# Kernel optimization log

Hardware: AMD Instinct MI355X
Metric: run time of the kernel (lower is better)

Reference implementation:

```python
import jax, jax.numpy as jnp
import numpy as np

V = 32000      # vocab_size
E = 256        # ModelConfig.n_embed
T_BLOCK = 2048 # ModelConfig.block_size
H = 4          # n_head (hardcoded in Bigram)
L = 3          # number of Blocks
HS = E // H    # head_size
EPS = 1e-5

def _ln(x, g, b):
    mu = jnp.mean(x, axis=-1, keepdims=True)
    var = jnp.var(x, axis=-1, keepdims=True)
    return (x - mu) * jax.lax.rsqrt(var + EPS) * g + b

def setup_inputs() -> dict:
    key = jax.random.key(0)
    ks = jax.random.split(key, 16)
    s = 0.02
    inp = {
        "idx": jax.random.randint(ks[0], (4, T_BLOCK), 0, V),
        "tok_emb": jax.random.normal(ks[1], (V, E), jnp.float32) * s,
        "pos_emb": jax.random.normal(ks[2], (T_BLOCK, E), jnp.float32) * s,
        # per-layer stacked params (heads concatenated -> full ExE projections)
        "Wq": jax.random.normal(ks[3], (L, E, E), jnp.float32) * s,
        "Wk": jax.random.normal(ks[4], (L, E, E), jnp.float32) * s,
        "Wv": jax.random.normal(ks[5], (L, E, E), jnp.float32) * s,
        "Wproj": jax.random.normal(ks[6], (L, E, E), jnp.float32) * s,
        "bproj": jnp.zeros((L, E), jnp.float32),
        "ln1_g": jnp.ones((L, E), jnp.float32),
        "ln1_b": jnp.zeros((L, E), jnp.float32),
        "W1": jax.random.normal(ks[7], (L, E, 4 * E), jnp.float32) * s,
        "b1": jnp.zeros((L, 4 * E), jnp.float32),
        "W2": jax.random.normal(ks[8], (L, 4 * E, E), jnp.float32) * s,
        "b2": jnp.zeros((L, E), jnp.float32),
        "ln2_g": jnp.ones((L, E), jnp.float32),
        "ln2_b": jnp.zeros((L, E), jnp.float32),
        "Wlm": jax.random.normal(ks[9], (E, V), jnp.float32) * s,
        "blm": jnp.zeros((V,), jnp.float32),
    }
    return inp

def reference(idx, tok_emb, pos_emb, Wq, Wk, Wv, Wproj, bproj, ln1_g, ln1_b,
              W1, b1, W2, b2, ln2_g, ln2_b, Wlm, blm):
    B, T = idx.shape
    x = tok_emb[idx] + pos_emb[:T]  # [B,T,E]
    causal = jnp.tril(jnp.ones((T, T), bool))
    # NOTE: source scales by C**0.5 with C = n_embed (not head_size)
    scale = 1.0 / jnp.sqrt(jnp.float32(E))
    for l in range(L):
        h = _ln(x, ln1_g[l], ln1_b[l])
        q = (h @ Wq[l]).reshape(B, T, H, HS).transpose(0, 2, 1, 3)
        k = (h @ Wk[l]).reshape(B, T, H, HS).transpose(0, 2, 1, 3)
        v = (h @ Wv[l]).reshape(B, T, H, HS).transpose(0, 2, 1, 3)
        wei = jnp.einsum('bhtd,bhsd->bhts', q, k) * scale
        wei = jnp.where(causal, wei, -jnp.inf)
        wei = jax.nn.softmax(wei, axis=-1)
        y = jnp.einsum('bhts,bhsd->bhtd', wei, v)
        y = y.transpose(0, 2, 1, 3).reshape(B, T, E)
        x = x + y @ Wproj[l] + bproj[l]
        h2 = _ln(x, ln2_g[l], ln2_b[l])
        x = x + jax.nn.relu(h2 @ W1[l] + b1[l]) @ W2[l] + b2[l]
    # ln_f exists in __init__ but is never applied in forward — skipped.
    logits = x @ Wlm + blm  # [B,T,V]
    return logits
```

## Files before the change

### kernel.cpp

```cpp
#include <hip/hip_runtime.h>
#include <hip/hip_bf16.h>

#define EMB 256
#define NHEAD 4
#define HSZ 64
#define NLAYER 3
#define TBLK 2048
#define VOCAB 32000
#define BATCH 4
#define LNEPS 1e-5f
#define BT (BATCH * TBLK)
#define QKVD (3 * EMB)

typedef __attribute__((ext_vector_type(8))) short bf16x8v;
typedef __attribute__((ext_vector_type(4))) float f32x4;
typedef unsigned short u16;
typedef unsigned int u32;

__device__ __forceinline__ u16 f2bf(float f) {
    union { float f; u32 u; } c; c.f = f;
    u32 r = c.u + 0x7fff + ((c.u >> 16) & 1);
    return (u16)(r >> 16);
}
__device__ __forceinline__ u32 pack2(float a, float b) {
    return (u32)f2bf(a) | ((u32)f2bf(b) << 16);
}

__global__ __launch_bounds__(64) void embed_kernel(
    const int* __restrict__ idx, const float* __restrict__ tok,
    const float* __restrict__ pos, float* __restrict__ x)
{
    const int row = blockIdx.x;
    const int t = row & (TBLK - 1);
    const int token = idx[row];
    const int e = threadIdx.x * 4;
    const float4 tv = *(const float4*)&tok[(size_t)token * EMB + e];
    const float4 pv = *(const float4*)&pos[(size_t)t * EMB + e];
    float4 o;
    o.x = tv.x + pv.x; o.y = tv.y + pv.y; o.z = tv.z + pv.z; o.w = tv.w + pv.w;
    *(float4*)&x[(size_t)row * EMB + e] = o;
}

__global__ __launch_bounds__(64) void ln_kernel(
    const float* __restrict__ x, const float* __restrict__ g,
    const float* __restrict__ b, u16* __restrict__ out)
{
    const int row = blockIdx.x;
    const int e = threadIdx.x * 4;
    const float4 xv = *(const float4*)&x[(size_t)row * EMB + e];
    float s1 = xv.x + xv.y + xv.z + xv.w;
    float s2 = xv.x * xv.x + xv.y * xv.y + xv.z * xv.z + xv.w * xv.w;
    #pragma unroll
    for (int off = 32; off >= 1; off >>= 1) {
        s1 += __shfl_xor(s1, off);
        s2 += __shfl_xor(s2, off);
    }
    const float mu  = s1 * (1.0f / EMB);
    const float var = s2 * (1.0f / EMB) - mu * mu;
    const float rs  = rsqrtf(var + LNEPS);
    const float4 gv = *(const float4*)&g[e];
    const float4 bv = *(const float4*)&b[e];
    ushort4 o;
    o.x = f2bf((xv.x - mu) * rs * gv.x + bv.x);
    o.y = f2bf((xv.y - mu) * rs * gv.y + bv.y);
    o.z = f2bf((xv.z - mu) * rs * gv.z + bv.z);
    o.w = f2bf((xv.w - mu) * rs * gv.w + bv.w);
    *(ushort4*)&out[(size_t)row * EMB + e] = o;
}

__global__ __launch_bounds__(256) void cast_kernel(
    const float* __restrict__ in, u16* __restrict__ out)
{
    const int i = (blockIdx.x * 256 + threadIdx.x) * 4;
    const float4 v = *(const float4*)&in[i];
    ushort4 o; o.x = f2bf(v.x); o.y = f2bf(v.y); o.z = f2bf(v.z); o.w = f2bf(v.w);
    *(ushort4*)&out[i] = o;
}

__global__ __launch_bounds__(256) void transpose_cast(
    const float* __restrict__ W, u16* __restrict__ Wt, int K, int N,
    size_t sW, size_t sWt)
{
    __shared__ float t[32][33];
    W  += (size_t)blockIdx.z * sW;
    Wt += (size_t)blockIdx.z * sWt;
    const int bx = blockIdx.x, by = blockIdx.y;
    const int tx = threadIdx.x, ty = threadIdx.y;
    #pragma unroll
    for (int i = 0; i < 32; i += 8)
        t[ty + i][tx] = W[(size_t)(by * 32 + ty + i) * N + bx * 32 + tx];
    __syncthreads();
    #pragma unroll
    for (int i = 0; i < 32; i += 8)
        Wt[(size_t)(bx * 32 + ty + i) * K + by * 32 + tx] = f2bf(t[tx][ty + i]);
}

template<int BNT, int BIAS, int RES, int RELU, int OUTBF>
__global__ __launch_bounds__(256) void mgemm(
    const u16* __restrict__ A, const u16* __restrict__ Bt,
    const float* __restrict__ bias, const float* __restrict__ res,
    void* __restrict__ Cv, int M, int N, int K)
{
    constexpr int LDW = 40;
    constexpr int MI = (BNT == 128) ? 4 : 2;
    __shared__ u16 Al[2][128 * LDW];
    __shared__ u16 Bl[2][BNT * LDW];
    const int tid = threadIdx.x;
    const int bm = blockIdx.x, bn = blockIdx.y;
    const int wid = tid >> 6, lane = tid & 63;
    const int wr = (BNT == 128) ? (wid >> 1) * 64 : wid * 32;
    const int wc = (BNT == 128) ? (wid & 1) * 64 : 0;
    const int fr = lane & 15, fq = lane >> 4;

    const int sra = tid >> 1,                       ska = (tid & 1) * 16;
    const int srb = (BNT == 128) ? (tid >> 1) : (tid >> 2);
    const int skb = (BNT == 128) ? (tid & 1) * 16 : (tid & 3) * 8;

    const u16* Ag = A + (size_t)(bm * 128 + sra) * K + ska;
    const u16* Bg = Bt + (size_t)(bn * BNT + srb) * K + skb;

    bf16x8v a0 = *(const bf16x8v*)Ag;
    bf16x8v a1 = *(const bf16x8v*)(Ag + 8);
    bf16x8v b0 = *(const bf16x8v*)Bg;
    bf16x8v b1 = (BNT == 128) ? *(const bf16x8v*)(Bg + 8) : b0;

    f32x4 acc[MI][4];
    #pragma unroll
    for (int i = 0; i < MI; ++i)
        #pragma unroll
        for (int j = 0; j < 4; ++j)
            acc[i][j] = f32x4{0.f, 0.f, 0.f, 0.f};

    int buf = 0;
    for (int k0 = 0; k0 < K; k0 += 32, buf ^= 1) {
        u16* Aw = &Al[buf][sra * LDW + ska];
        *(bf16x8v*)Aw = a0; *(bf16x8v*)(Aw + 8) = a1;
        u16* Bw = &Bl[buf][srb * LDW + skb];
        *(bf16x8v*)Bw = b0;
        if (BNT == 128) *(bf16x8v*)(Bw + 8) = b1;
        __syncthreads();
        if (k0 + 32 < K) {
            a0 = *(const bf16x8v*)(Ag + k0 + 32);
            a1 = *(const bf16x8v*)(Ag + k0 + 40);
            b0 = *(const bf16x8v*)(Bg + k0 + 32);
            if (BNT == 128) b1 = *(const bf16x8v*)(Bg + k0 + 40);
        }
        bf16x8v af[MI], bfr[4];
        #pragma unroll
        for (int mi = 0; mi < MI; ++mi)
            af[mi] = *(const bf16x8v*)&Al[buf][(wr + mi * 16 + fr) * LDW + fq * 8];
        #pragma unroll
        for (int ni = 0; ni < 4; ++ni)
            bfr[ni] = *(const bf16x8v*)&Bl[buf][(wc + ni * 16 + fr) * LDW + fq * 8];
        #pragma unroll
        for (int mi = 0; mi < MI; ++mi)
            #pragma unroll
            for (int ni = 0; ni < 4; ++ni)
                acc[mi][ni] = __builtin_amdgcn_mfma_f32_16x16x32_bf16(
                    af[mi], bfr[ni], acc[mi][ni], 0, 0, 0);
    }

    float* Cf = (float*)Cv;
    u16*   Cb = (u16*)Cv;
    #pragma unroll
    for (int mi = 0; mi < MI; ++mi) {
        #pragma unroll
        for (int j = 0; j < 4; ++j) {
            const int r = bm * 128 + wr + mi * 16 + fq * 4 + j;
            #pragma unroll
            for (int ni = 0; ni < 4; ++ni) {
                const int c = bn * BNT + wc + ni * 16 + fr;
                float v = acc[mi][ni][j];
                if (BIAS) v += bias[c];
                if (RELU) v = fmaxf(v, 0.f);
                if (RES)  v += res[(size_t)r * N + c];
                if (OUTBF) Cb[(size_t)r * N + c] = f2bf(v);
                else       Cf[(size_t)r * N + c] = v;
            }
        }
    }
}

__global__ __launch_bounds__(256) void attn_kernel(
    const u16* __restrict__ qkv, u16* __restrict__ y)
{
    constexpr int LDK = 72;
    __shared__ u16 Kl[2][64 * LDK];
    __shared__ u16 Vt[2][64 * LDK];

    const int tid = threadIdx.x;
    const int qt = (int)gridDim.x - 1 - (int)blockIdx.x;
    const int bh = blockIdx.y;
    const int b = bh >> 2, h = bh & 3;
    const int w = tid >> 6, lane = tid & 63;
    const int fr = lane & 15, fq = lane >> 4;
    const size_t rowbase = (size_t)b * TBLK;
    const int qoff = h * HSZ, koff = EMB + h * HSZ, voff = 2 * EMB + h * HSZ;
    const int qg = qt * 64 + w * 16 + fr;

    bf16x8v qf[2];
    #pragma unroll
    for (int ks = 0; ks < 2; ++ks)
        qf[ks] = *(const bf16x8v*)&qkv[(rowbase + qg) * QKVD + qoff + ks * 32 + fq * 8];

    f32x4 yac[4];
    #pragma unroll
    for (int mi = 0; mi < 4; ++mi) yac[mi] = f32x4{0.f, 0.f, 0.f, 0.f};
    float m = -1e30f, l = 0.f;

    const int skv = tid >> 2, sc = (tid & 3) * 16;
    const u16* kbase = &qkv[(rowbase + skv) * QKVD + koff + sc];
    const u16* vbase = &qkv[(rowbase + skv) * QKVD + voff + sc];

    bf16x8v kr0 = *(const bf16x8v*)kbase;
    bf16x8v kr1 = *(const bf16x8v*)(kbase + 8);
    bf16x8v vr0 = *(const bf16x8v*)vbase;
    bf16x8v vr1 = *(const bf16x8v*)(vbase + 8);

    int buf = 0;
    for (int kv0 = 0; kv0 <= qt * 64; kv0 += 64, buf ^= 1) {
        {
            u16* Kw = &Kl[buf][skv * LDK + sc];
            *(bf16x8v*)Kw = kr0; *(bf16x8v*)(Kw + 8) = kr1;
            #pragma unroll
            for (int i = 0; i < 8; ++i) Vt[buf][(sc + i) * LDK + skv] = (u16)vr0[i];
            #pragma unroll
            for (int i = 0; i < 8; ++i) Vt[buf][(sc + 8 + i) * LDK + skv] = (u16)vr1[i];
        }
        __syncthreads();
        if (kv0 + 64 <= qt * 64) {
            const size_t off = (size_t)(kv0 + 64) * QKVD;
            kr0 = *(const bf16x8v*)(kbase + off);
            kr1 = *(const bf16x8v*)(kbase + off + 8);
            vr0 = *(const bf16x8v*)(vbase + off);
            vr1 = *(const bf16x8v*)(vbase + off + 8);
        }

        f32x4 st[4];
        #pragma unroll
        for (int mb = 0; mb < 4; ++mb) {
            st[mb] = f32x4{0.f, 0.f, 0.f, 0.f};
            #pragma unroll
            for (int ks = 0; ks < 2; ++ks) {
                const bf16x8v kf = *(const bf16x8v*)
                    &Kl[buf][(mb * 16 + fr) * LDK + ks * 32 + fq * 8];
                st[mb] = __builtin_amdgcn_mfma_f32_16x16x32_bf16(
                    kf, qf[ks], st[mb], 0, 0, 0);
            }
        }
        float p[4][4];
        float mloc = -1e30f;
        #pragma unroll
        for (int mb = 0; mb < 4; ++mb)
            #pragma unroll
            for (int j = 0; j < 4; ++j) {
                const int kvg = kv0 + mb * 16 + fq * 4 + j;
                const float s = (kvg <= qg) ? st[mb][j] * 0.0625f : -1e30f;
                p[mb][j] = s;
                mloc = fmaxf(mloc, s);
            }
        mloc = fmaxf(mloc, __shfl_xor(mloc, 16));
        mloc = fmaxf(mloc, __shfl_xor(mloc, 32));
        const float mnew = fmaxf(m, mloc);
        const float alpha = __expf(m - mnew);
        float rsum = 0.f;
        #pragma unroll
        for (int mb = 0; mb < 4; ++mb)
            #pragma unroll
            for (int j = 0; j < 4; ++j) {
                p[mb][j] = __expf(p[mb][j] - mnew);
                rsum += p[mb][j];
            }
        rsum += __shfl_xor(rsum, 16);
        rsum += __shfl_xor(rsum, 32);
        l = l * alpha + rsum;
        m = mnew;
        #pragma unroll
        for (int mi = 0; mi < 4; ++mi) yac[mi] *= alpha;

        u32 pk[4][2];
        #pragma unroll
        for (int mb = 0; mb < 4; ++mb) {
            pk[mb][0] = pack2(p[mb][0], p[mb][1]);
            pk[mb][1] = pack2(p[mb][2], p[mb][3]);
        }
        #pragma unroll
        for (int ksv = 0; ksv < 2; ++ksv) {
            union { u32 u[4]; bf16x8v v; } pf;
            #pragma unroll
            for (int t = 0; t < 4; ++t) {
                const int srcl = ((fq & 1) * 2 + (t >> 1)) * 16 + fr;
                const u32 lo = __shfl(pk[ksv * 2 + 0][t & 1], srcl);
                const u32 hi = __shfl(pk[ksv * 2 + 1][t & 1], srcl);
                pf.u[t] = (fq >> 1) ? hi : lo;
            }
            #pragma unroll
            for (int mi = 0; mi < 4; ++mi) {
                const bf16x8v vf = *(const bf16x8v*)
                    &Vt[buf][(mi * 16 + fr) * LDK + ksv * 32 + fq * 8];
                yac[mi] = __builtin_amdgcn_mfma_f32_16x16x32_bf16(
                    vf, pf.v, yac[mi], 0, 0, 0);
            }
        }
    }

    const float inv = 1.f / l;
    #pragma unroll
    for (int mi = 0; mi < 4; ++mi) {
        ushort4 o;
        o.x = f2bf(yac[mi][0] * inv);
        o.y = f2bf(yac[mi][1] * inv);
        o.z = f2bf(yac[mi][2] * inv);
        o.w = f2bf(yac[mi][3] * inv);
        *(ushort4*)&y[(rowbase + qg) * EMB + h * HSZ + mi * 16 + fq * 4] = o;
    }
}

extern "C" void kernel_launch(void* const* d_in, const int* in_sizes, int n_in,
                              void* d_out, int out_size, void* d_ws, size_t ws_size,
                              hipStream_t stream) {
    const int*   idx   = (const int*)  d_in[0];
    const float* tok   = (const float*)d_in[1];
    const float* pos   = (const float*)d_in[2];
    const float* Wq    = (const float*)d_in[3];
    const float* Wk    = (const float*)d_in[4];
    const float* Wv    = (const float*)d_in[5];
    const float* Wproj = (const float*)d_in[6];
    const float* bproj = (const float*)d_in[7];
    const float* ln1g  = (const float*)d_in[8];
    const float* ln1b  = (const float*)d_in[9];
    const float* W1    = (const float*)d_in[10];
    const float* b1    = (const float*)d_in[11];
    const float* W2    = (const float*)d_in[12];
    const float* b2    = (const float*)d_in[13];
    const float* ln2g  = (const float*)d_in[14];
    const float* ln2b  = (const float*)d_in[15];
    const float* Wlm   = (const float*)d_in[16];
    const float* blm   = (const float*)d_in[17];
    float* out = (float*)d_out;

    float* x    = (float*)d_ws;
    u16*   hb   = (u16*)(x + (size_t)BT * EMB);
    u16*   qkvb = hb + (size_t)BT * EMB;
    u16*   yb   = qkvb + (size_t)BT * QKVD;
    u16*   hid  = qkvb;
    u16*   Wqkvt  = yb + (size_t)BT * EMB;
    u16*   Wprojt = Wqkvt  + (size_t)NLAYER * QKVD * EMB;
    u16*   W1t    = Wprojt + (size_t)NLAYER * EMB * EMB;
    u16*   W2t    = W1t    + (size_t)NLAYER * EMB * 4 * EMB;
    u16*   Wlmt   = W2t    + (size_t)NLAYER * 4 * EMB * EMB;

    const dim3 tb(32, 8);
    transpose_cast<<<dim3(8, 8, NLAYER), tb, 0, stream>>>(
        Wq, Wqkvt, EMB, EMB, (size_t)EMB*EMB, (size_t)QKVD*EMB);
    transpose_cast<<<dim3(8, 8, NLAYER), tb, 0, stream>>>(
        Wk, Wqkvt + EMB*EMB, EMB, EMB, (size_t)EMB*EMB, (size_t)QKVD*EMB);
    transpose_cast<<<dim3(8, 8, NLAYER), tb, 0, stream>>>(
        Wv, Wqkvt + 2*EMB*EMB, EMB, EMB, (size_t)EMB*EMB, (size_t)QKVD*EMB);
    transpose_cast<<<dim3(8, 8, NLAYER), tb, 0, stream>>>(
        Wproj, Wprojt, EMB, EMB, (size_t)EMB*EMB, (size_t)EMB*EMB);
    transpose_cast<<<dim3(32, 8, NLAYER), tb, 0, stream>>>(
        W1, W1t, EMB, 4*EMB, (size_t)EMB*4*EMB, (size_t)EMB*4*EMB);
    transpose_cast<<<dim3(8, 32, NLAYER), tb, 0, stream>>>(
        W2, W2t, 4*EMB, EMB, (size_t)4*EMB*EMB, (size_t)4*EMB*EMB);
    transpose_cast<<<dim3(VOCAB/32, 8, 1), tb, 0, stream>>>(
        Wlm, Wlmt, EMB, VOCAB, 0, 0);

    embed_kernel<<<BT, 64, 0, stream>>>(idx, tok, pos, x);

    for (int l = 0; l < NLAYER; ++l) {
        ln_kernel<<<BT, 64, 0, stream>>>(x, ln1g + l*EMB, ln1b + l*EMB, hb);
        mgemm<128,0,0,0,1><<<dim3(BT/128, QKVD/128), 256, 0, stream>>>(
            hb, Wqkvt + (size_t)l*QKVD*EMB, nullptr, nullptr, qkvb, BT, QKVD, EMB);
        attn_kernel<<<dim3(TBLK/64, BATCH*NHEAD), 256, 0, stream>>>(qkvb, yb);
        mgemm<64,1,1,0,0><<<dim3(BT/128, EMB/64), 256, 0, stream>>>(
            yb, Wprojt + (size_t)l*EMB*EMB, bproj + l*EMB, x, x, BT, EMB, EMB);
        ln_kernel<<<BT, 64, 0, stream>>>(x, ln2g + l*EMB, ln2b + l*EMB, hb);
        mgemm<128,1,0,1,1><<<dim3(BT/128, 4*EMB/128), 256, 0, stream>>>(
            hb, W1t + (size_t)l*EMB*4*EMB, b1 + l*4*EMB, nullptr, hid, BT, 4*EMB, EMB);
        mgemm<64,1,1,0,0><<<dim3(BT/128, EMB/64), 256, 0, stream>>>(
            hid, W2t + (size_t)l*4*EMB*EMB, b2 + l*EMB, x, x, BT, EMB, 4*EMB);
    }

    cast_kernel<<<BT*EMB/1024, 256, 0, stream>>>(x, hb);
    mgemm<128,1,0,0,0><<<dim3(BT/128, VOCAB/128), 256, 0, stream>>>(
        hb, Wlmt, blm, nullptr, out, BT, VOCAB, EMB);
}
```

Baseline: 710.4 us.

## Use direct global-to-LDS loads in GEMM, add MFMA priority, fuse small launches

The GEMM staging now uses global_load_lds to copy A/B tiles straight into unpadded LDS, replacing the register round-trip and padded stores. MFMA sections in the GEMM and attention kernels are wrapped with s_setprio. Several small launches are merged: the QKV/proj weight transposes become one kernel, embed/LN pack four rows per block, and the final cast is folded into the last W2 GEMM with bf16 output. Dropping the LDS padding may bring back bank conflicts on fragment reads.

Result: no change. 701.0 us (-1.3%).

```diff
diff --git a/kernel.cpp b/kernel.cpp
--- a/kernel.cpp
+++ b/kernel.cpp
@@ -26,14 +26,20 @@
     return (u32)f2bf(a) | ((u32)f2bf(b) << 16);
 }
 
-__global__ __launch_bounds__(64) void embed_kernel(
+__device__ __forceinline__ void gload16(const u16* g, u16* l) {
+    __builtin_amdgcn_global_load_lds(
+        (__attribute__((address_space(1))) void*)g,
+        (__attribute__((address_space(3))) void*)l, 16, 0, 0);
+}
+
+__global__ __launch_bounds__(256) void embed_kernel(
     const int* __restrict__ idx, const float* __restrict__ tok,
     const float* __restrict__ pos, float* __restrict__ x)
 {
-    const int row = blockIdx.x;
+    const int row = blockIdx.x * 4 + (threadIdx.x >> 6);
     const int t = row & (TBLK - 1);
     const int token = idx[row];
-    const int e = threadIdx.x * 4;
+    const int e = (threadIdx.x & 63) * 4;
     const float4 tv = *(const float4*)&tok[(size_t)token * EMB + e];
     const float4 pv = *(const float4*)&pos[(size_t)t * EMB + e];
     float4 o;
@@ -41,12 +47,12 @@
     *(float4*)&x[(size_t)row * EMB + e] = o;
 }
 
-__global__ __launch_bounds__(64) void ln_kernel(
+__global__ __launch_bounds__(256) void ln_kernel(
     const float* __restrict__ x, const float* __restrict__ g,
     const float* __restrict__ b, u16* __restrict__ out)
 {
-    const int row = blockIdx.x;
-    const int e = threadIdx.x * 4;
+    const int row = blockIdx.x * 4 + (threadIdx.x >> 6);
+    const int e = (threadIdx.x & 63) * 4;
     const float4 xv = *(const float4*)&x[(size_t)row * EMB + e];
     float s1 = xv.x + xv.y + xv.z + xv.w;
     float s2 = xv.x * xv.x + xv.y * xv.y + xv.z * xv.z + xv.w * xv.w;
@@ -68,15 +74,6 @@
     *(ushort4*)&out[(size_t)row * EMB + e] = o;
 }
 
-__global__ __launch_bounds__(256) void cast_kernel(
-    const float* __restrict__ in, u16* __restrict__ out)
-{
-    const int i = (blockIdx.x * 256 + threadIdx.x) * 4;
-    const float4 v = *(const float4*)&in[i];
-    ushort4 o; o.x = f2bf(v.x); o.y = f2bf(v.y); o.z = f2bf(v.z); o.w = f2bf(v.w);
-    *(ushort4*)&out[i] = o;
-}
-
 __global__ __launch_bounds__(256) void transpose_cast(
     const float* __restrict__ W, u16* __restrict__ Wt, int K, int N,
     size_t sW, size_t sWt)
@@ -95,16 +92,41 @@
         Wt[(size_t)(bx * 32 + ty + i) * K + by * 32 + tx] = f2bf(t[tx][ty + i]);
 }
 
+__global__ __launch_bounds__(256) void transpose_qkvp(
+    const float* __restrict__ Wq, const float* __restrict__ Wk,
+    const float* __restrict__ Wv, const float* __restrict__ Wp,
+    u16* __restrict__ Wqkvt, u16* __restrict__ Wprojt)
+{
+    __shared__ float t[32][33];
+    const int which = blockIdx.z & 3, l = blockIdx.z >> 2;
+    const float* W;
+    u16* Wt;
+    switch (which) {
+        case 0: W = Wq + (size_t)l*EMB*EMB; Wt = Wqkvt + (size_t)l*QKVD*EMB;               break;
+        case 1: W = Wk + (size_t)l*EMB*EMB; Wt = Wqkvt + (size_t)l*QKVD*EMB + EMB*EMB;     break;
+        case 2: W = Wv + (size_t)l*EMB*EMB; Wt = Wqkvt + (size_t)l*QKVD*EMB + 2*EMB*EMB;   break;
+        default:W = Wp + (size_t)l*EMB*EMB; Wt = Wprojt + (size_t)l*EMB*EMB;               break;
+    }
+    const int bx = blockIdx.x, by = blockIdx.y;
+    const int tx = threadIdx.x, ty = threadIdx.y;
+    #pragma unroll
+    for (int i = 0; i < 32; i += 8)
+        t[ty + i][tx] = W[(size_t)(by * 32 + ty + i) * EMB + bx * 32 + tx];
+    __syncthreads();
+    #pragma unroll
+    for (int i = 0; i < 32; i += 8)
+        Wt[(size_t)(bx * 32 + ty + i) * EMB + by * 32 + tx] = f2bf(t[tx][ty + i]);
+}
+
 template<int BNT, int BIAS, int RES, int RELU, int OUTBF>
 __global__ __launch_bounds__(256) void mgemm(
     const u16* __restrict__ A, const u16* __restrict__ Bt,
     const float* __restrict__ bias, const float* __restrict__ res,
     void* __restrict__ Cv, int M, int N, int K)
 {
-    constexpr int LDW = 40;
     constexpr int MI = (BNT == 128) ? 4 : 2;
-    __shared__ u16 Al[2][128 * LDW];
-    __shared__ u16 Bl[2][BNT * LDW];
+    __shared__ u16 Al[2][128 * 32];
+    __shared__ u16 Bl[2][BNT * 32];
     const int tid = threadIdx.x;
     const int bm = blockIdx.x, bn = blockIdx.y;
     const int wid = tid >> 6, lane = tid & 63;
@@ -112,17 +134,10 @@
     const int wc = (BNT == 128) ? (wid & 1) * 64 : 0;
     const int fr = lane & 15, fq = lane >> 4;
 
-    const int sra = tid >> 1,                       ska = (tid & 1) * 16;
-    const int srb = (BNT == 128) ? (tid >> 1) : (tid >> 2);
-    const int skb = (BNT == 128) ? (tid & 1) * 16 : (tid & 3) * 8;
-
-    const u16* Ag = A + (size_t)(bm * 128 + sra) * K + ska;
-    const u16* Bg = Bt + (size_t)(bn * BNT + srb) * K + skb;
-
-    bf16x8v a0 = *(const bf16x8v*)Ag;
-    bf16x8v a1 = *(const bf16x8v*)(Ag + 8);
-    bf16x8v b0 = *(const bf16x8v*)Bg;
-    bf16x8v b1 = (BNT == 128) ? *(const bf16x8v*)(Bg + 8) : b0;
+    const int l4 = lane >> 2, lc = (lane & 3) * 8;
+    const u16* Aga = A  + (size_t)(bm * 128 + wid * 16 + l4) * K + lc;
+    const u16* Bga = Bt + (size_t)(bn * BNT + wid * 16 + l4) * K + lc;
+    const int lin = (wid * 16 + l4) * 32 + lc;
 
     f32x4 acc[MI][4];
     #pragma unroll
@@ -131,33 +146,36 @@
         for (int j = 0; j < 4; ++j)
             acc[i][j] = f32x4{0.f, 0.f, 0.f, 0.f};
 
+    gload16(Aga,                  &Al[0][lin]);
+    gload16(Aga + (size_t)64 * K, &Al[0][lin + 64 * 32]);
+    gload16(Bga,                  &Bl[0][lin]);
+    if (BNT == 128) gload16(Bga + (size_t)64 * K, &Bl[0][lin + 64 * 32]);
+
     int buf = 0;
     for (int k0 = 0; k0 < K; k0 += 32, buf ^= 1) {
-        u16* Aw = &Al[buf][sra * LDW + ska];
-        *(bf16x8v*)Aw = a0; *(bf16x8v*)(Aw + 8) = a1;
-        u16* Bw = &Bl[buf][srb * LDW + skb];
-        *(bf16x8v*)Bw = b0;
-        if (BNT == 128) *(bf16x8v*)(Bw + 8) = b1;
         __syncthreads();
         if (k0 + 32 < K) {
-            a0 = *(const bf16x8v*)(Ag + k0 + 32);
-            a1 = *(const bf16x8v*)(Ag + k0 + 40);
-            b0 = *(const bf16x8v*)(Bg + k0 + 32);
-            if (BNT == 128) b1 = *(const bf16x8v*)(Bg + k0 + 40);
+            gload16(Aga + k0 + 32,                  &Al[buf ^ 1][lin]);
+            gload16(Aga + (size_t)64 * K + k0 + 32, &Al[buf ^ 1][lin + 64 * 32]);
+            gload16(Bga + k0 + 32,                  &Bl[buf ^ 1][lin]);
+            if (BNT == 128)
+                gload16(Bga + (size_t)64 * K + k0 + 32, &Bl[buf ^ 1][lin + 64 * 32]);
         }
         bf16x8v af[MI], bfr[4];
         #pragma unroll
         for (int mi = 0; mi < MI; ++mi)
-            af[mi] = *(const bf16x8v*)&Al[buf][(wr + mi * 16 + fr) * LDW + fq * 8];
+            af[mi] = *(const bf16x8v*)&Al[buf][(wr + mi * 16 + fr) * 32 + fq * 8];
         #pragma unroll
         for (int ni = 0; ni < 4; ++ni)
-            bfr[ni] = *(const bf16x8v*)&Bl[buf][(wc + ni * 16 + fr) * LDW + fq * 8];
+            bfr[ni] = *(const bf16x8v*)&Bl[buf][(wc + ni * 16 + fr) * 32 + fq * 8];
+        __builtin_amdgcn_s_setprio(1);
         #pragma unroll
         for (int mi = 0; mi < MI; ++mi)
             #pragma unroll
             for (int ni = 0; ni < 4; ++ni)
                 acc[mi][ni] = __builtin_amdgcn_mfma_f32_16x16x32_bf16(
                     af[mi], bfr[ni], acc[mi][ni], 0, 0, 0);
+        __builtin_amdgcn_s_setprio(0);
     }
 
     float* Cf = (float*)Cv;
@@ -237,6 +255,7 @@
         }
 
         f32x4 st[4];
+        __builtin_amdgcn_s_setprio(1);
         #pragma unroll
         for (int mb = 0; mb < 4; ++mb) {
             st[mb] = f32x4{0.f, 0.f, 0.f, 0.f};
@@ -248,6 +267,7 @@
                     kf, qf[ks], st[mb], 0, 0, 0);
             }
         }
+        __builtin_amdgcn_s_setprio(0);
         float p[4][4];
         float mloc = -1e30f;
         #pragma unroll
@@ -294,6 +314,7 @@
                 const u32 hi = __shfl(pk[ksv * 2 + 1][t & 1], srcl);
                 pf.u[t] = (fq >> 1) ? hi : lo;
             }
+            __builtin_amdgcn_s_setprio(1);
             #pragma unroll
             for (int mi = 0; mi < 4; ++mi) {
                 const bf16x8v vf = *(const bf16x8v*)
@@ -301,6 +322,7 @@
                 yac[mi] = __builtin_amdgcn_mfma_f32_16x16x32_bf16(
                     vf, pf.v, yac[mi], 0, 0, 0);
             }
+            __builtin_amdgcn_s_setprio(0);
         }
     }
 
@@ -351,14 +373,8 @@
     u16*   Wlmt   = W2t    + (size_t)NLAYER * 4 * EMB * EMB;
 
     const dim3 tb(32, 8);
-    transpose_cast<<<dim3(8, 8, NLAYER), tb, 0, stream>>>(
-        Wq, Wqkvt, EMB, EMB, (size_t)EMB*EMB, (size_t)QKVD*EMB);
-    transpose_cast<<<dim3(8, 8, NLAYER), tb, 0, stream>>>(
-        Wk, Wqkvt + EMB*EMB, EMB, EMB, (size_t)EMB*EMB, (size_t)QKVD*EMB);
-    transpose_cast<<<dim3(8, 8, NLAYER), tb, 0, stream>>>(
-        Wv, Wqkvt + 2*EMB*EMB, EMB, EMB, (size_t)EMB*EMB, (size_t)QKVD*EMB);
-    transpose_cast<<<dim3(8, 8, NLAYER), tb, 0, stream>>>(
-        Wproj, Wprojt, EMB, EMB, (size_t)EMB*EMB, (size_t)EMB*EMB);
+    transpose_qkvp<<<dim3(8, 8, NLAYER * 4), tb, 0, stream>>>(
+        Wq, Wk, Wv, Wproj, Wqkvt, Wprojt);
     transpose_cast<<<dim3(32, 8, NLAYER), tb, 0, stream>>>(
         W1, W1t, EMB, 4*EMB, (size_t)EMB*4*EMB, (size_t)EMB*4*EMB);
     transpose_cast<<<dim3(8, 32, NLAYER), tb, 0, stream>>>(
@@ -366,23 +382,27 @@
     transpose_cast<<<dim3(VOCAB/32, 8, 1), tb, 0, stream>>>(
         Wlm, Wlmt, EMB, VOCAB, 0, 0);
 
-    embed_kernel<<<BT, 64, 0, stream>>>(idx, tok, pos, x);
+    embed_kernel<<<BT/4, 256, 0, stream>>>(idx, tok, pos, x);
 
     for (int l = 0; l < NLAYER; ++l) {
-        ln_kernel<<<BT, 64, 0, stream>>>(x, ln1g + l*EMB, ln1b + l*EMB, hb);
+        ln_kernel<<<BT/4, 256, 0, stream>>>(x, ln1g + l*EMB, ln1b + l*EMB, hb);
         mgemm<128,0,0,0,1><<<dim3(BT/128, QKVD/128), 256, 0, stream>>>(
             hb, Wqkvt + (size_t)l*QKVD*EMB, nullptr, nullptr, qkvb, BT, QKVD, EMB);
         attn_kernel<<<dim3(TBLK/64, BATCH*NHEAD), 256, 0, stream>>>(qkvb, yb);
         mgemm<64,1,1,0,0><<<dim3(BT/128, EMB/64), 256, 0, stream>>>(
             yb, Wprojt + (size_t)l*EMB*EMB, bproj + l*EMB, x, x, BT, EMB, EMB);
-        ln_kernel<<<BT, 64, 0, stream>>>(x, ln2g + l*EMB, ln2b + l*EMB, hb);
+        ln_kernel<<<BT/4, 256, 0, stream>>>(x, ln2g + l*EMB, ln2b + l*EMB, hb);
         mgemm<128,1,0,1,1><<<dim3(BT/128, 4*EMB/128), 256, 0, stream>>>(
             hb, W1t + (size_t)l*EMB*4*EMB, b1 + l*4*EMB, nullptr, hid, BT, 4*EMB, EMB);
-        mgemm<64,1,1,0,0><<<dim3(BT/128, EMB/64), 256, 0, stream>>>(
-            hid, W2t + (size_t)l*4*EMB*EMB, b2 + l*EMB, x, x, BT, EMB, 4*EMB);
-    }
-
-    cast_kernel<<<BT*EMB/1024, 256, 0, stream>>>(x, hb);
+        if (l < NLAYER - 1) {
+            mgemm<64,1,1,0,0><<<dim3(BT/128, EMB/64), 256, 0, stream>>>(
+                hid, W2t + (size_t)l*4*EMB*EMB, b2 + l*EMB, x, x, BT, EMB, 4*EMB);
+        } else {
+            mgemm<64,1,1,0,1><<<dim3(BT/128, EMB/64), 256, 0, stream>>>(
+                hid, W2t + (size_t)l*4*EMB*EMB, b2 + l*EMB, x, hb, BT, EMB, 4*EMB);
+        }
+    }
+
     mgemm<128,1,0,0,0><<<dim3(BT/128, VOCAB/128), 256, 0, stream>>>(
         hb, Wlmt, blm, nullptr, out, BT, VOCAB, EMB);
 }
```
